# Kernel tuning notes

Measured on AMD Instinct MI355X. Metric: run time of the kernel, lower is better.

The kernel has to match this reference:

```python
import jax
import jax.numpy as jnp
import numpy as np
from jax import lax


def _extrema_mask(x):
    # x: (W,). Mirrors the torch diff/pad/sign logic exactly.
    dx = x[1:] - x[:-1]
    right = jnp.pad(dx, (0, 1)) > 0          # F.pad(dx,[0,1]) > 0
    left = jnp.pad(dx, (1, 0)) <= 0          # F.pad(dx,[1,0]) <= 0
    s = (1 - jnp.sign(x)).astype(bool)       # True where x <= 0
    valleys = right & left & s
    peaks = (~right) & (~left) & (~s)
    return peaks | valleys


def _suppress_one(x, dist):
    # x: (W,) single signal. Greedy NMS-like suppression over extrema
    # sorted by |value| descending.
    W = x.shape[0]
    e = _extrema_mask(x)
    key = jnp.where(e, jnp.abs(x), -jnp.inf)  # non-extrema sort last
    order = jnp.argsort(-key)                 # descending by |x| among extrema
    pos = order                               # original positions, sorted
    valid = e[order]                          # padded (non-extrema) entries

    def step(is_sec, i):
        act = valid[i] & (~is_sec[i])
        within = (pos >= pos[i] - dist) & (pos <= pos[i] + dist)
        new = jnp.where(act, is_sec | within, is_sec)
        new = new.at[i].set(jnp.where(act, False, new[i]))
        return new, None

    is_sec, _ = lax.scan(step, jnp.zeros(W, dtype=bool), jnp.arange(W))
    primary = valid & (~is_sec)
    # pos is a permutation of 0..W-1, so scatter-set is exact
    out = jnp.zeros_like(x).at[pos].set(jnp.where(primary, x[pos], 0.0))
    return out


def setup_inputs() -> dict:
    key = jax.random.key(0)
    x = jax.random.normal(key, (128, 1, 4096), dtype=jnp.float32)
    return {"x": x, "minimum_extrema_distance": 32}


def reference(x, minimum_extrema_distance):
    B, C, W = x.shape  # C == 1 as assumed by the original module
    flat = x.reshape(B * C, W)
    out = jax.vmap(lambda s: _suppress_one(s, minimum_extrema_distance))(flat)
    return out.reshape(B, C, W)
```

## Files before the change

kernel.cpp:

```cpp
#include <hip/hip_runtime.h>

typedef unsigned long long u64;
typedef unsigned int u32;

#define W    4096
#define NT   128
#define CH   32
#define NCH  128
#define D32  32
#define PSTR 33
#define PSH  ((NCH + 4) * PSTR)

#define PFXI(c, o) (((c) + 2) * PSTR + (o))
#define SFXI(c, o) (PSH + ((c) + 2) * PSTR + (o))

__global__ __launch_bounds__(NT) void extrema_nms_ps(
    const float* __restrict__ x,
    const int*   __restrict__ dist_p,
    float*       __restrict__ out)
{
    const int sig = blockIdx.x;
    const float* xg = x + (size_t)sig * W;
    float*       og = out + (size_t)sig * W;
    const int dist = *dist_p;

    __shared__ __align__(16) float xs[W];
    __shared__ __align__(16) u64   HMb[NCH + 4];
    __shared__ __align__(16) u32   PS[2 * PSH];
    __shared__ int LF;

    const int tid = threadIdx.x;

    {
        const float4* xg4 = (const float4*)xg;
        float4*       xs4 = (float4*)xs;
        #pragma unroll
        for (int v = tid; v < W / 4; v += NT) xs4[v] = xg4[v];
    }
    for (int k = tid; k < 4 * PSTR; k += NT) {
        const int rr = k / PSTR, oo = k % PSTR;
        const int row = (rr < 2) ? rr : (NCH + rr);
        PS[row * PSTR + oo] = 0u;
        PS[PSH + row * PSTR + oo] = 0u;
    }
    if (tid < 2) { HMb[tid] = 0ull; HMb[NCH + 2 + tid] = 0ull; }
    if (tid == 0) LF = 0;
    __syncthreads();

    if (dist == D32) {
        const int base = tid * CH;

        u32 kb[CH];
        {
            const float4* xs4 = (const float4*)xs;
            float f[CH + 2];
            #pragma unroll
            for (int v = 0; v < 8; ++v) {
                const float4 q = xs4[tid * 8 + v];
                f[4 * v + 1] = q.x; f[4 * v + 2] = q.y;
                f[4 * v + 3] = q.z; f[4 * v + 4] = q.w;
            }
            f[0]      = (tid > 0)      ? xs[base - 1]  : __int_as_float(0x7f800000);
            f[CH + 1] = (tid < NT - 1) ? xs[base + CH] : f[CH];
            #pragma unroll
            for (int j = 0; j < CH; ++j) {
                const float xi = f[j + 1];
                const bool right = f[j + 2] > xi;
                const bool left  = xi <= f[j];
                const bool s     = xi <= 0.0f;
                const bool ext   = (right && left && s) || (!right && !left && !s);
                const u32 ab = __float_as_uint(xi) & 0x7fffffffu;
                kb[j] = ext ? ((ab << 1) | 1u) : 0u;
            }
        }
        u32 L = 0;
        #pragma unroll
        for (int j = 0; j < CH; ++j) if (kb[j]) L |= (1u << j);
        u32 best = 0; int bo = 0;
        #pragma unroll
        for (int j = 0; j < CH; ++j) if (kb[j] > best) { best = kb[j]; bo = j; }

        #define PUBLISH()                                                      \
        do {                                                                   \
            u32 m_ = 0;                                                        \
            _Pragma("unroll")                                                  \
            for (int j = 0; j < CH; ++j) {                                     \
                const u32 kj = ((L >> j) & 1u) ? kb[j] : 0u;                   \
                m_ = kj > m_ ? kj : m_;                                        \
                PS[PFXI(tid, j)] = m_;                                         \
            }                                                                  \
            m_ = 0;                                                            \
            _Pragma("unroll")                                                  \
            for (int j = CH - 1; j >= 0; --j) {                                \
                const u32 kj = ((L >> j) & 1u) ? kb[j] : 0u;                   \
                m_ = kj > m_ ? kj : m_;                                        \
                PS[SFXI(tid, j)] = m_;                                         \
            }                                                                  \
            HMb[tid + 2] = best ? (((u64)best << 32) | (u32)(base + bo)) : 0ull; \
        } while (0)

        PUBLISH();
        int kpos = -1;

        int r = 0;
        for (;;) {
            ++r;
            const u64 bal = __ballot(best != 0u);
            if ((tid & 63) == 0 && bal) LF = r;
            __syncthreads();
            const int live = LF;
            const u64 hL = HMb[tid + 1];
            const u64 hR = HMb[tid + 3];
            if (live != r) break;

            bool keep_c = false, keep_m = false, keep_p = false;
            int pL = 0, pR = 0;
            if (best) {
                const u32 sl = PS[SFXI(tid - 1, bo)];
                const u32 pr = PS[PFXI(tid + 1, bo)];
                keep_c = (sl < best) && (pr <= best);
            }
            const u32 ML = (u32)(hL >> 32);
            if (ML) {
                pL = (int)(u32)hL;
                const int boL = pL - base + CH;
                const u32 sl = PS[SFXI(tid - 2, boL)];
                const u32 pr = PS[PFXI(tid,     boL)];
                keep_m = (sl < ML) && (pr <= ML);
            }
            const u32 MR = (u32)(hR >> 32);
            if (MR) {
                pR = (int)(u32)hR;
                const int boR = pR - base - CH;
                const u32 sl = PS[SFXI(tid,     boR)];
                const u32 pr = PS[PFXI(tid + 2, boR)];
                keep_p = (sl < MR) && (pr <= MR);
            }
            __syncthreads();

            u32 newL = L;
            if (keep_m) { const int boL = pL - base + CH; newL &= ~(0xFFFFFFFFu >> (31 - boL)); }
            if (keep_p) { const int boR = pR - base - CH; newL &= ~(0xFFFFFFFFu << boR); }
            if (keep_c) { newL = 0u; kpos = bo; }

            if (newL != L) {
                L = newL;
                if (best && !((L >> bo) & 1u)) {
                    best = 0; bo = 0;
                    #pragma unroll
                    for (int j = 0; j < CH; ++j) {
                        const u32 kj = ((L >> j) & 1u) ? kb[j] : 0u;
                        if (kj > best) { best = kj; bo = j; }
                    }
                }
                PUBLISH();
            }
        }

        {
            const float4* xs4 = (const float4*)xs;
            float4*       og4 = (float4*)og;
            #pragma unroll
            for (int v = 0; v < 8; ++v) {
                const float4 q = xs4[tid * 8 + v];
                const int j0 = 4 * v;
                float4 o;
                o.x = (kpos == j0 + 0) ? q.x : 0.0f;
                o.y = (kpos == j0 + 1) ? q.y : 0.0f;
                o.z = (kpos == j0 + 2) ? q.z : 0.0f;
                o.w = (kpos == j0 + 3) ? q.w : 0.0f;
                og4[tid * 8 + v] = o;
            }
        }
    } else {
        u64* SK = (u64*)PS;
        for (int i = tid; i < W; i += NT) og[i] = 0.0f;
        for (int i = tid; i < W; i += NT) {
            const float xi = xs[i];
            const bool right = (i < W - 1) ? (xs[i + 1] > xi) : false;
            const bool left  = (i > 0)     ? (xi <= xs[i - 1]) : true;
            const bool s = (xi <= 0.0f);
            const bool valley = right && left && s;
            const bool peak   = !right && !left && !s;
            const u32 ab = __float_as_uint(xi) & 0x7fffffffu;
            SK[i] = (valley || peak) ? (((u64)ab << 32) | (u64)(u32)(W - 1 - i)) : 0ull;
        }
        __syncthreads();

        for (;;) {
            u64 m = 0ull;
            #pragma unroll
            for (int j = 0; j < W / NT; ++j) {
                const u64 k = SK[tid + j * NT];
                if (k > m) m = k;
            }
            #pragma unroll
            for (int off = 32; off > 0; off >>= 1) {
                const u64 o = __shfl_down(m, off, 64);
                if (o > m) m = o;
            }
            if ((tid & 63) == 0) HMb[tid >> 6] = m;
            __syncthreads();
            if (tid == 0) HMb[0] = (HMb[1] > HMb[0]) ? HMb[1] : HMb[0];
            __syncthreads();
            const u64 win = HMb[0];
            if (win == 0ull) break;

            const int p = (W - 1) - (int)(win & 0xffffffffu);
            if (tid == 0) og[p] = xs[p];

            int lo = p - dist; lo = lo < 0 ? 0 : lo;
            int hi = p + dist; hi = hi > (W - 1) ? (W - 1) : hi;
            for (int j = lo + tid; j <= hi; j += NT) SK[j] = 0ull;
            __syncthreads();
        }
    }
}

extern "C" void kernel_launch(void* const* d_in, const int* in_sizes, int n_in,
                              void* d_out, int out_size, void* d_ws, size_t ws_size,
                              hipStream_t stream) {
    const float* x      = (const float*)d_in[0];
    const int*   dist_p = (const int*)d_in[1];
    float*       out    = (float*)d_out;
    const int nsig = in_sizes[0] / W;
    hipLaunchKernelGGL(extrema_nms_ps, dim3(nsig), dim3(NT), 0, stream,
                       x, dist_p, out);
}
```

Before: 17.48 us.

## Replace neighbor candidate checks with kept-position broadcast in single-barrier rounds

Restructures the dist==32 suppression loop. Each chunk now checks only its own best candidate against neighbouring prefix/suffix maxima. When kept, it writes the kept position into a small KEPT array that neighbouring chunks read to mask out positions within the distance. This removes the second barrier per round and the redundant evaluation of neighbours' candidates. The cost is that a kill may take one extra round to propagate, since neighbours read KEPT one round later.

```diff
diff --git a/kernel.cpp b/kernel.cpp
--- a/kernel.cpp
+++ b/kernel.cpp
@@ -10,11 +10,10 @@
 #define D32  32
 #define PSTR 33
 #define PSH  ((NCH + 4) * PSTR)
-
 #define PFXI(c, o) (((c) + 2) * PSTR + (o))
 #define SFXI(c, o) (PSH + ((c) + 2) * PSTR + (o))
 
-__global__ __launch_bounds__(NT) void extrema_nms_ps(
+__global__ __launch_bounds__(NT) void extrema_nms_sb(
     const float* __restrict__ x,
     const int*   __restrict__ dist_p,
     float*       __restrict__ out)
@@ -25,9 +24,10 @@
     const int dist = *dist_p;
 
     __shared__ __align__(16) float xs[W];
-    __shared__ __align__(16) u64   HMb[NCH + 4];
     __shared__ __align__(16) u32   PS[2 * PSH];
-    __shared__ int LF;
+    __shared__ u32   KEPT[NCH + 2];
+    __shared__ int   LF;
+    __shared__ u64   red[2];
 
     const int tid = threadIdx.x;
 
@@ -43,12 +43,13 @@
         PS[row * PSTR + oo] = 0u;
         PS[PSH + row * PSTR + oo] = 0u;
     }
-    if (tid < 2) { HMb[tid] = 0ull; HMb[NCH + 2 + tid] = 0ull; }
+    if (tid < NCH + 2 - NT) KEPT[NT + tid] = 0u;
+    KEPT[tid] = 0u;
     if (tid == 0) LF = 0;
     __syncthreads();
 
     if (dist == D32) {
-        const int base = tid * CH;
+        const int c = tid, base = tid * CH;
 
         u32 kb[CH];
         {
@@ -73,87 +74,78 @@
                 kb[j] = ext ? ((ab << 1) | 1u) : 0u;
             }
         }
-        u32 L = 0;
+        u32 P = 0;
         #pragma unroll
-        for (int j = 0; j < CH; ++j) if (kb[j]) L |= (1u << j);
+        for (int j = 0; j < CH; ++j) if (kb[j]) P |= (1u << j);
         u32 best = 0; int bo = 0;
         #pragma unroll
         for (int j = 0; j < CH; ++j) if (kb[j] > best) { best = kb[j]; bo = j; }
 
-        #define PUBLISH()                                                      \
+        #define PUBLISH(m)                                                     \
         do {                                                                   \
-            u32 m_ = 0;                                                        \
+            u32 a_ = 0;                                                        \
             _Pragma("unroll")                                                  \
             for (int j = 0; j < CH; ++j) {                                     \
-                const u32 kj = ((L >> j) & 1u) ? kb[j] : 0u;                   \
-                m_ = kj > m_ ? kj : m_;                                        \
-                PS[PFXI(tid, j)] = m_;                                         \
+                const u32 kj = (((m) >> j) & 1u) ? kb[j] : 0u;                 \
+                a_ = kj > a_ ? kj : a_;                                        \
+                PS[PFXI(c, j)] = a_;                                           \
             }                                                                  \
-            m_ = 0;                                                            \
+            a_ = 0;                                                            \
             _Pragma("unroll")                                                  \
             for (int j = CH - 1; j >= 0; --j) {                                \
-                const u32 kj = ((L >> j) & 1u) ? kb[j] : 0u;                   \
-                m_ = kj > m_ ? kj : m_;                                        \
-                PS[SFXI(tid, j)] = m_;                                         \
+                const u32 kj = (((m) >> j) & 1u) ? kb[j] : 0u;                 \
+                a_ = kj > a_ ? kj : a_;                                        \
+                PS[SFXI(c, j)] = a_;                                           \
             }                                                                  \
-            HMb[tid + 2] = best ? (((u64)best << 32) | (u32)(base + bo)) : 0ull; \
         } while (0)
 
-        PUBLISH();
+        PUBLISH(P);
         int kpos = -1;
 
-        int r = 0;
-        for (;;) {
-            ++r;
-            const u64 bal = __ballot(best != 0u);
+        for (int r = 1;; ++r) {
+            const u64 bal = __ballot(P != 0u);
             if ((tid & 63) == 0 && bal) LF = r;
             __syncthreads();
-            const int live = LF;
-            const u64 hL = HMb[tid + 1];
-            const u64 hR = HMb[tid + 3];
-            if (live != r) break;
-
-            bool keep_c = false, keep_m = false, keep_p = false;
-            int pL = 0, pR = 0;
-            if (best) {
-                const u32 sl = PS[SFXI(tid - 1, bo)];
-                const u32 pr = PS[PFXI(tid + 1, bo)];
-                keep_c = (sl < best) && (pr <= best);
-            }
-            const u32 ML = (u32)(hL >> 32);
-            if (ML) {
-                pL = (int)(u32)hL;
-                const int boL = pL - base + CH;
-                const u32 sl = PS[SFXI(tid - 2, boL)];
-                const u32 pr = PS[PFXI(tid,     boL)];
-                keep_m = (sl < ML) && (pr <= ML);
-            }
-            const u32 MR = (u32)(hR >> 32);
-            if (MR) {
-                pR = (int)(u32)hR;
-                const int boR = pR - base - CH;
-                const u32 sl = PS[SFXI(tid,     boR)];
-                const u32 pr = PS[PFXI(tid + 2, boR)];
-                keep_p = (sl < MR) && (pr <= MR);
-            }
-            __syncthreads();
-
-            u32 newL = L;
-            if (keep_m) { const int boL = pL - base + CH; newL &= ~(0xFFFFFFFFu >> (31 - boL)); }
-            if (keep_p) { const int boR = pR - base - CH; newL &= ~(0xFFFFFFFFu << boR); }
-            if (keep_c) { newL = 0u; kpos = bo; }
-
-            if (newL != L) {
-                L = newL;
-                if (best && !((L >> bo) & 1u)) {
-                    best = 0; bo = 0;
-                    #pragma unroll
-                    for (int j = 0; j < CH; ++j) {
-                        const u32 kj = ((L >> j) & 1u) ? kb[j] : 0u;
-                        if (kj > best) { best = kj; bo = j; }
+            if (LF != r) break;
+
+            if (P) {
+                const u32 sl  = PS[SFXI(c - 1, bo)];
+                const u32 pr  = PS[PFXI(c + 1, bo)];
+                const u32 kmL = KEPT[c];
+                const u32 kmR = KEPT[c + 2];
+
+                const bool keep_c = (sl < best) && (pr <= best);
+                if (keep_c) {
+                    KEPT[c + 1] = (u32)(base + bo + 1);
+                    kpos = bo;
+                    P = 0u;
+                    PUBLISH(1u << bo);
+                } else {
+                    u32 killwin = 0u;
+                    if (kmL) {
+                        const int e = (int)kmL - 1 - base + D32;
+                        if (e >= 31) killwin = 0xffffffffu;
+                        else if (e >= 0) killwin = (1u << (e + 1)) - 1u;
+                    }
+                    if (kmR) {
+                        const int s2 = (int)kmR - 1 - base - D32;
+                        if (s2 <= 0) killwin = 0xffffffffu;
+                        else if (s2 <= 31) killwin |= (0xffffffffu << s2);
+                    }
+                    const u32 newP = P & ~killwin;
+                    if (newP != P) {
+                        P = newP;
+                        if (!((P >> bo) & 1u)) {
+                            best = 0; bo = 0;
+                            #pragma unroll
+                            for (int j = 0; j < CH; ++j) {
+                                const u32 kj = ((P >> j) & 1u) ? kb[j] : 0u;
+                                if (kj > best) { best = kj; bo = j; }
+                            }
+                        }
+                        PUBLISH(P);
                     }
                 }
-                PUBLISH();
             }
         }
 
@@ -165,7 +157,7 @@
                 const float4 q = xs4[tid * 8 + v];
                 const int j0 = 4 * v;
                 float4 o;
-                o.x = (kpos == j0 + 0) ? q.x : 0.0f;
+                o.x = (kpos == j0    ) ? q.x : 0.0f;
                 o.y = (kpos == j0 + 1) ? q.y : 0.0f;
                 o.z = (kpos == j0 + 2) ? q.z : 0.0f;
                 o.w = (kpos == j0 + 3) ? q.w : 0.0f;
@@ -199,11 +191,11 @@
                 const u64 o = __shfl_down(m, off, 64);
                 if (o > m) m = o;
             }
-            if ((tid & 63) == 0) HMb[tid >> 6] = m;
-            __syncthreads();
-            if (tid == 0) HMb[0] = (HMb[1] > HMb[0]) ? HMb[1] : HMb[0];
-            __syncthreads();
-            const u64 win = HMb[0];
+            if ((tid & 63) == 0) red[tid >> 6] = m;
+            __syncthreads();
+            if (tid == 0 && red[1] > red[0]) red[0] = red[1];
+            __syncthreads();
+            const u64 win = red[0];
             if (win == 0ull) break;
 
             const int p = (W - 1) - (int)(win & 0xffffffffu);
@@ -224,6 +216,6 @@
     const int*   dist_p = (const int*)d_in[1];
     float*       out    = (float*)d_out;
     const int nsig = in_sizes[0] / W;
-    hipLaunchKernelGGL(extrema_nms_ps, dim3(nsig), dim3(NT), 0, stream,
+    hipLaunchKernelGGL(extrema_nms_sb, dim3(nsig), dim3(NT), 0, stream,
                        x, dist_p, out);
 }
```

Measured after the change: 24.23 us. +38.6%, slower.
